# Kernel optimization log

Hardware: AMD Instinct MI355X
Metric: run time of the kernel (lower is better)

## Reference

```python
import jax, jax.numpy as jnp
import numpy as np
import math

NUM_HEADS = 32
NUM_KV_HEADS = 8
HEAD_DIM = 64
ROPE_THETA = 150000.0


def rotate_half(x):
    half = x.shape[-1] // 2
    return jnp.concatenate([-x[..., half:], x[..., :half]], axis=-1)


def setup_inputs() -> dict:
    key = jax.random.key(0)
    k1, k2, k3, k4, k5 = jax.random.split(key, 5)
    B, S, H = 2, 2048, 2048
    qkv_size = (NUM_HEADS + 2 * NUM_KV_HEADS) * HEAD_DIM  # 3072
    scale = 1.0 / math.sqrt(H)
    return {
        "hidden_states": jax.random.normal(k1, (B, S, H), jnp.float32),
        "position_ids": jnp.arange(S, dtype=jnp.int64 if jax.config.jax_enable_x64 else jnp.int32)[None, :],
        "qkv_w": jax.random.normal(k2, (qkv_size, H), jnp.float32) * scale,
        "qkv_b": jax.random.normal(k3, (qkv_size,), jnp.float32) * 0.01,
        "o_w": jax.random.normal(k4, (H, NUM_HEADS * HEAD_DIM), jnp.float32) * scale,
        "o_b": jax.random.normal(k5, (H,), jnp.float32) * 0.01,
    }


def reference(hidden_states, position_ids, qkv_w, qkv_b, o_w, o_b):
    B, S, _ = hidden_states.shape
    g = NUM_HEADS // NUM_KV_HEADS  # query heads per kv head
    d = HEAD_DIM

    qkv = hidden_states @ qkv_w.T + qkv_b  # [B,S,(H+2KV)*d]
    qkv = qkv.reshape(B, S, NUM_KV_HEADS, g + 2, d)
    q = qkv[:, :, :, :g, :].reshape(B, S, NUM_HEADS, d).transpose(0, 2, 1, 3)   # [B,Hq,S,d]
    k = qkv[:, :, :, g, :].transpose(0, 2, 1, 3)                                 # [B,Hkv,S,d]
    v = qkv[:, :, :, g + 1, :].transpose(0, 2, 1, 3)                             # [B,Hkv,S,d]

    # HF-style RoPE: cos/sin [S, d]
    inv_freq = 1.0 / (ROPE_THETA ** (jnp.arange(0, d, 2, dtype=jnp.float32) / d))
    freqs = jnp.outer(position_ids.reshape(-1).astype(jnp.float32), inv_freq)    # [S, d/2]
    emb = jnp.concatenate([freqs, freqs], axis=-1)                               # [S, d]
    cos = jnp.cos(emb)[None, None]                                               # [1,1,S,d]
    sin = jnp.sin(emb)[None, None]
    q = q * cos + rotate_half(q) * sin
    k = k * cos + rotate_half(k) * sin

    # GQA: repeat_interleave kv heads to match query heads
    k = jnp.repeat(k, g, axis=1)  # [B,Hq,S,d]
    v = jnp.repeat(v, g, axis=1)

    scores = jnp.einsum("bhqd,bhkd->bhqk", q, k) / math.sqrt(d)  # [B,Hq,S,S]
    attn = jax.nn.softmax(scores, axis=-1)
    out = jnp.einsum("bhqk,bhkd->bhqd", attn, v)
    out = out.transpose(0, 2, 1, 3).reshape(B, S, NUM_HEADS * d)
    return out @ o_w.T + o_b
```

## Files before the change

kernel.cpp:

```cpp
#include <hip/hip_runtime.h>
#include <math.h>

#define NHQ 32
#define NKV 8
#define HD 64
#define QKV_DIM 3072
#define MODEL_DIM 2048
#define QSCALE 0.1803368801111204f

typedef __attribute__((ext_vector_type(4))) float     f32x4;
typedef __attribute__((ext_vector_type(8))) _Float16  half8;
typedef __attribute__((ext_vector_type(4))) _Float16  half4v;
typedef __attribute__((ext_vector_type(2))) __fp16    fp16x2;
typedef __attribute__((ext_vector_type(4))) unsigned  uint32x4;

#define ASYNC_COPY16(g, l)                                                        \
    __builtin_amdgcn_global_load_lds(                                             \
        (const __attribute__((address_space(1))) void*)(g),                       \
        (__attribute__((address_space(3))) void*)(l), 16, 0, 0)

__device__ __forceinline__ float fast_exp2(float x)
{
#if __has_builtin(__builtin_amdgcn_exp2f)
    return __builtin_amdgcn_exp2f(x);
#else
    float r;
    asm volatile("v_exp_f32 %0, %1\ns_nop 0" : "=v"(r) : "v"(x));
    return r;
#endif
}

__global__ __launch_bounds__(256)
void f32_to_f16_kernel(const float* __restrict__ src, _Float16* __restrict__ dst, int n4)
{
    int i = blockIdx.x * 256 + threadIdx.x;
    if (i < n4) {
        float4 v = ((const float4*)src)[i];
        half4v h = { (_Float16)v.x, (_Float16)v.y, (_Float16)v.z, (_Float16)v.w };
        ((half4v*)dst)[i] = h;
    }
}

__global__ __launch_bounds__(256)
void sincos_table_kernel(const int* __restrict__ pos, float* __restrict__ tab, int S)
{
    int i = blockIdx.x * 256 + threadIdx.x;
    if (i < S * 32) {
        int s = i >> 5, fi = i & 31;
        float p = (float)pos[s];
        float inv_freq = powf(150000.0f, -(float)fi * (1.0f / 32.0f));
        float ang = p * inv_freq;
        tab[s * 64 + fi]      = cosf(ang);
        tab[s * 64 + 32 + fi] = sinf(ang);
    }
}

template<int MODE>
__global__ __launch_bounds__(512, 2)
void gemm_f16_mfma(const _Float16* __restrict__ A, const _Float16* __restrict__ W,
                   const float* __restrict__ bias, void* __restrict__ Cout,
                   const float* __restrict__ tab, int M, int N, int K, int S)
{
    __shared__ _Float16 As[3][128 * 32];
    __shared__ _Float16 Bs[3][256 * 32];

    const int t    = threadIdx.x;
    const int w    = t >> 6;
    const int lane = t & 63;
    const int quad = lane >> 4, l15 = lane & 15;
    const size_t m0 = (size_t)blockIdx.y * 128;
    const size_t n0 = (size_t)blockIdx.x * 256;
    const int wm = (w >> 2) * 64;
    const int wn = (w & 3) * 64;

    const int sr   = t >> 2;
    const int klog = ((t & 3) ^ ((sr >> 1) & 3)) * 8;
    const _Float16* ag0 = A + (m0 + sr) * K + klog;
    const _Float16* bg0 = W + (n0 + sr) * K + klog;
    const _Float16* bg1 = W + (n0 + 128 + sr) * K + klog;

    const int xk8 = (quad ^ ((l15 >> 1) & 3)) * 8;

    f32x4 acc[4][4];
#pragma unroll
    for (int i = 0; i < 4; i++)
#pragma unroll
        for (int j = 0; j < 4; j++) acc[i][j] = (f32x4){0.f, 0.f, 0.f, 0.f};

    const int nkt = K >> 5;

#define STAGE_TILE(bi, kt_)                                         \
    do {                                                            \
        const int _k0 = (kt_) * 32;                                 \
        ASYNC_COPY16(ag0 + _k0, &As[bi][w * 512]);                  \
        ASYNC_COPY16(bg0 + _k0, &Bs[bi][w * 512]);                  \
        ASYNC_COPY16(bg1 + _k0, &Bs[bi][4096 + w * 512]);           \
    } while (0)

    STAGE_TILE(0, 0);
    STAGE_TILE(1, 1);
    asm volatile("s_waitcnt vmcnt(3)" ::: "memory");
    __builtin_amdgcn_s_barrier();
    __builtin_amdgcn_sched_barrier(0);

    int bc = 0;
    for (int kt = 0; kt < nkt; ++kt) {
        const _Float16* Ab = &As[bc][0];
        const _Float16* Bb = &Bs[bc][0];

        half8 af[4], bf[4];
#pragma unroll
        for (int i = 0; i < 4; i++) {
            af[i] = *(const half8*)(Ab + (wm + i * 16 + l15) * 32 + xk8);
            bf[i] = *(const half8*)(Bb + (wn + i * 16 + l15) * 32 + xk8);
        }

        if (kt + 2 < nkt) {
            int bs = bc + 2; if (bs >= 3) bs -= 3;
            STAGE_TILE(bs, kt + 2);
        }

        __builtin_amdgcn_s_setprio(1);
#pragma unroll
        for (int i = 0; i < 4; i++)
#pragma unroll
            for (int j = 0; j < 4; j++)
                acc[i][j] = __builtin_amdgcn_mfma_f32_16x16x32_f16(af[i], bf[j], acc[i][j], 0, 0, 0);
        __builtin_amdgcn_s_setprio(0);

        if (kt + 1 < nkt) {
            if (kt + 2 < nkt) asm volatile("s_waitcnt vmcnt(3)" ::: "memory");
            else              asm volatile("s_waitcnt vmcnt(0)" ::: "memory");
            __builtin_amdgcn_s_barrier();
            __builtin_amdgcn_sched_barrier(0);
        }
        bc = bc + 1; if (bc == 3) bc = 0;
    }
#undef STAGE_TILE

    float bv[4];
#pragma unroll
    for (int j = 0; j < 4; j++) bv[j] = bias[n0 + wn + j * 16 + l15];

    const int ct = (int)(((n0 + wn) >> 6) % 6);

#pragma unroll
    for (int i = 0; i < 4; i++)
#pragma unroll
        for (int r = 0; r < 4; r++) {
            const size_t row = m0 + wm + i * 16 + quad * 4 + r;
            float v[4];
#pragma unroll
            for (int j = 0; j < 4; j++) v[j] = acc[i][j][r] + bv[j];

            if (MODE == 2 && ct != 5) {
                const float* tc = tab + (size_t)(row % S) * 64;
                const float ca = tc[l15],      sa = tc[32 + l15];
                const float cb = tc[16 + l15], sb = tc[48 + l15];
                const float qs = (ct < 4) ? QSCALE : 1.0f;
                const float n0v = v[0] * ca - v[2] * sa;
                const float n1v = v[1] * cb - v[3] * sb;
                const float n2v = v[2] * ca + v[0] * sa;
                const float n3v = v[3] * cb + v[1] * sb;
                v[0] = n0v * qs; v[1] = n1v * qs; v[2] = n2v * qs; v[3] = n3v * qs;
            }

            const size_t col = n0 + wn + l15;
#pragma unroll
            for (int j = 0; j < 4; j++) {
                if (MODE != 0) ((_Float16*)Cout)[row * N + col + j * 16] = (_Float16)v[j];
                else           ((float*)Cout)[row * N + col + j * 16] = v[j];
            }
        }
}

__global__ __launch_bounds__(256)
void transpose_v_kernel(const _Float16* __restrict__ qkv, _Float16* __restrict__ vtg, int BS)
{
    __shared__ _Float16 tile[64 * 72];
    const int t = threadIdx.x;
    const int tb = blockIdx.x * 64;
    const int g = blockIdx.y;
    const int voff = (g * 6 + 5) * 64;

    const int tok = t >> 2, dsub = (t & 3) * 16;
    const _Float16* src = qkv + (size_t)(tb + tok) * QKV_DIM + voff + dsub;
    *(half8*)&tile[tok * 72 + dsub]     = *(const half8*)(src);
    *(half8*)&tile[tok * 72 + dsub + 8] = *(const half8*)(src + 8);
    __syncthreads();

    const int d = t >> 2, tsub = (t & 3) * 16;
    half8 a, c;
#pragma unroll
    for (int i = 0; i < 8; i++) a[i] = tile[(tsub + i) * 72 + d];
#pragma unroll
    for (int i = 0; i < 8; i++) c[i] = tile[(tsub + 8 + i) * 72 + d];
    _Float16* dst = vtg + ((size_t)g * 64 + d) * BS + tb + tsub;
    *(half8*)dst       = a;
    *(half8*)(dst + 8) = c;
}

__global__ __launch_bounds__(256)
void attn_mfma(const _Float16* __restrict__ qkv, const _Float16* __restrict__ vtg,
               _Float16* __restrict__ out, int B, int S)
{
    __shared__ _Float16 Ks[64 * 72];
    __shared__ _Float16 VsT[64 * 72];

    const int t = threadIdx.x, w = t >> 6, lane = t & 63;
    const int quad = lane >> 4, l15 = lane & 15;
    const int b = blockIdx.z, g = blockIdx.y;
    const int q0 = blockIdx.x * 32;
    const int qoff = (g * 6 + w) * 64;
    const int koff = (g * 6 + 4) * 64;

    half8 qf[2][2];
#pragma unroll
    for (int s = 0; s < 2; s++) {
        const _Float16* qp = qkv + (size_t)(b * S + q0 + s * 16 + l15) * QKV_DIM + qoff;
        qf[s][0] = *(const half8*)(qp + quad * 8);
        qf[s][1] = *(const half8*)(qp + 32 + quad * 8);
    }

    half8 lv;
    {
        const _Float16 one = (l15 == 0) ? (_Float16)1.0f : (_Float16)0.0f;
#pragma unroll
        for (int j = 0; j < 8; j++) lv[j] = one;
    }

    f32x4 O[2][4], L[2];
#pragma unroll
    for (int s = 0; s < 2; s++) {
        L[s] = (f32x4){0.f, 0.f, 0.f, 0.f};
#pragma unroll
        for (int dt = 0; dt < 4; dt++) O[s][dt] = (f32x4){0.f, 0.f, 0.f, 0.f};
    }

    const int kst_tok = t >> 2;
    const int kst_d   = (t & 3) * 16;
    const int vst_d   = t >> 3;
    const int vst_sub = (t & 7) * 8;

    const _Float16* kbase  = qkv + (size_t)(b * S + kst_tok) * QKV_DIM + koff + kst_d;
    const _Float16* vbase0 = vtg + ((size_t)g * 64 + vst_d) * (size_t)(B * S) + b * S + vst_sub;
    const _Float16* vbase1 = vtg + ((size_t)g * 64 + 32 + vst_d) * (size_t)(B * S) + b * S + vst_sub;

    half8 kr0 = *(const half8*)(kbase);
    half8 kr1 = *(const half8*)(kbase + 8);
    half8 vr0 = *(const half8*)(vbase0);
    half8 vr1 = *(const half8*)(vbase1);

    for (int kt = 0; kt < S; kt += 64) {
        *(half8*)&Ks[kst_tok * 72 + kst_d]         = kr0;
        *(half8*)&Ks[kst_tok * 72 + kst_d + 8]     = kr1;
        *(half8*)&VsT[vst_d * 72 + vst_sub]        = vr0;
        *(half8*)&VsT[(32 + vst_d) * 72 + vst_sub] = vr1;
        __syncthreads();

        if (kt + 64 < S) {
            kr0 = *(const half8*)(kbase + (size_t)(kt + 64) * QKV_DIM);
            kr1 = *(const half8*)(kbase + (size_t)(kt + 64) * QKV_DIM + 8);
            vr0 = *(const half8*)(vbase0 + kt + 64);
            vr1 = *(const half8*)(vbase1 + kt + 64);
        }

        half8 kf[4][2];
#pragma unroll
        for (int mt = 0; mt < 4; mt++) {
            kf[mt][0] = *(const half8*)&Ks[(mt * 16 + l15) * 72 + quad * 8];
            kf[mt][1] = *(const half8*)&Ks[(mt * 16 + l15) * 72 + 32 + quad * 8];
        }

        half8 pf[2][2];
#pragma unroll
        for (int s = 0; s < 2; s++) {
            f32x4 sacc[4];
#pragma unroll
            for (int mt = 0; mt < 4; mt++) {
                f32x4 z = (f32x4){0.f, 0.f, 0.f, 0.f};
                z = __builtin_amdgcn_mfma_f32_16x16x32_f16(kf[mt][0], qf[s][0], z, 0, 0, 0);
                z = __builtin_amdgcn_mfma_f32_16x16x32_f16(kf[mt][1], qf[s][1], z, 0, 0, 0);
                sacc[mt] = z;
            }

            unsigned u[4][2];
#pragma unroll
            for (int mt = 0; mt < 4; mt++) {
                fp16x2 pa = __builtin_amdgcn_cvt_pkrtz(fast_exp2(sacc[mt][0]),
                                                       fast_exp2(sacc[mt][1]));
                fp16x2 pb = __builtin_amdgcn_cvt_pkrtz(fast_exp2(sacc[mt][2]),
                                                       fast_exp2(sacc[mt][3]));
                u[mt][0] = __builtin_bit_cast(unsigned, pa);
                u[mt][1] = __builtin_bit_cast(unsigned, pb);
            }

#pragma unroll
            for (int h = 0; h < 2; h++) {
                uint32x4 pw;
#pragma unroll
                for (int c = 0; c < 2; c++) {
                    unsigned x = u[h * 2][c], y = u[h * 2 + 1][c];
                    asm("v_permlane32_swap_b32 %0, %1" : "+v"(x), "+v"(y));
                    asm("v_permlane16_swap_b32 %0, %1" : "+v"(x), "+v"(y));
                    pw[c]     = x;
                    pw[2 + c] = y;
                }
                pf[s][h] = __builtin_bit_cast(half8, pw);
            }
        }

#pragma unroll
        for (int dt = 0; dt < 4; dt++) {
            half8 vv0 = *(const half8*)&VsT[(dt * 16 + l15) * 72 + quad * 8];
            half8 vv1 = *(const half8*)&VsT[(dt * 16 + l15) * 72 + 32 + quad * 8];
#pragma unroll
            for (int s = 0; s < 2; s++) {
                O[s][dt] = __builtin_amdgcn_mfma_f32_16x16x32_f16(pf[s][0], vv0, O[s][dt], 0, 0, 0);
                O[s][dt] = __builtin_amdgcn_mfma_f32_16x16x32_f16(pf[s][1], vv1, O[s][dt], 0, 0, 0);
            }
        }
#pragma unroll
        for (int s = 0; s < 2; s++) {
            L[s] = __builtin_amdgcn_mfma_f32_16x16x32_f16(pf[s][0], lv, L[s], 0, 0, 0);
            L[s] = __builtin_amdgcn_mfma_f32_16x16x32_f16(pf[s][1], lv, L[s], 0, 0, 0);
        }
        __syncthreads();
    }

    const int hq = g * 4 + w;
#pragma unroll
    for (int s = 0; s < 2; s++)
#pragma unroll
        for (int r = 0; r < 4; r++) {
            const float lr = __shfl(L[s][r], lane & 48, 64);
            const float ir = 1.0f / lr;
            const size_t row = (size_t)(b * S + q0 + s * 16 + quad * 4 + r);
#pragma unroll
            for (int dt = 0; dt < 4; dt++)
                out[row * (NHQ * HD) + hq * 64 + dt * 16 + l15] = (_Float16)(O[s][dt][r] * ir);
        }
}

extern "C" void kernel_launch(void* const* d_in, const int* in_sizes, int n_in,
                              void* d_out, int out_size, void* d_ws, size_t ws_size,
                              hipStream_t stream)
{
    const float* hidden = (const float*)d_in[0];
    const int*   pos    = (const int*)d_in[1];
    const float* qkv_w  = (const float*)d_in[2];
    const float* qkv_b  = (const float*)d_in[3];
    const float* o_w    = (const float*)d_in[4];
    const float* o_b    = (const float*)d_in[5];
    float* out = (float*)d_out;

    const int S  = in_sizes[1];
    const int BS = in_sizes[0] / MODEL_DIM;
    const int B  = BS / S;

    _Float16* hA   = (_Float16*)d_ws;
    _Float16* hW1  = hA   + (size_t)BS * MODEL_DIM;
    _Float16* hW2  = hW1  + (size_t)QKV_DIM * MODEL_DIM;
    _Float16* qkvh = hW2  + (size_t)MODEL_DIM * MODEL_DIM;
    _Float16* atth = qkvh + (size_t)BS * QKV_DIM;
    float*    tab  = (float*)(atth + (size_t)BS * MODEL_DIM);
    _Float16* vtg  = (_Float16*)(tab + (size_t)S * 64);

    f32_to_f16_kernel<<<(BS * MODEL_DIM / 4 + 255) / 256, 256, 0, stream>>>(hidden, hA, BS * MODEL_DIM / 4);
    f32_to_f16_kernel<<<(QKV_DIM * MODEL_DIM / 4 + 255) / 256, 256, 0, stream>>>(qkv_w, hW1, QKV_DIM * MODEL_DIM / 4);
    f32_to_f16_kernel<<<(MODEL_DIM * MODEL_DIM / 4 + 255) / 256, 256, 0, stream>>>(o_w, hW2, MODEL_DIM * MODEL_DIM / 4);
    sincos_table_kernel<<<(S * 32 + 255) / 256, 256, 0, stream>>>(pos, tab, S);

    gemm_f16_mfma<2><<<dim3(QKV_DIM / 256, BS / 128), 512, 0, stream>>>(
        hA, hW1, qkv_b, qkvh, tab, BS, QKV_DIM, MODEL_DIM, S);

    transpose_v_kernel<<<dim3(BS / 64, NKV), 256, 0, stream>>>(qkvh, vtg, BS);

    attn_mfma<<<dim3(S / 32, NKV, B), 256, 0, stream>>>(qkvh, vtg, atth, B, S);

    gemm_f16_mfma<0><<<dim3(MODEL_DIM / 256, BS / 128), 512, 0, stream>>>(
        atth, hW2, o_b, out, nullptr, BS, MODEL_DIM, MODEL_DIM, S);
}
```

Before: 315.7 us.

## Enlarge GEMM tile to 256x256x64 with phased double-buffered staging; fuse prep kernels

New measurement: 339.5 us. +7.6%, slower.

```diff
diff --git a/kernel.cpp b/kernel.cpp
--- a/kernel.cpp
+++ b/kernel.cpp
@@ -31,27 +31,30 @@
 }
 
 __global__ __launch_bounds__(256)
-void f32_to_f16_kernel(const float* __restrict__ src, _Float16* __restrict__ dst, int n4)
-{
-    int i = blockIdx.x * 256 + threadIdx.x;
-    if (i < n4) {
-        float4 v = ((const float4*)src)[i];
+void prep_kernel(const float* __restrict__ s0, _Float16* __restrict__ d0, int n0,
+                 const float* __restrict__ s1, _Float16* __restrict__ d1, int n1,
+                 const float* __restrict__ s2, _Float16* __restrict__ d2, int n2,
+                 const int* __restrict__ pos, float* __restrict__ tab, int ns)
+{
+    int j = blockIdx.x * 256 + threadIdx.x;
+    if (j < n0 + n1 + n2) {
+        const float* s; _Float16* d;
+        if (j < n0)           { s = s0; d = d0; }
+        else if (j < n0 + n1) { s = s1; d = d1; j -= n0; }
+        else                  { s = s2; d = d2; j -= n0 + n1; }
+        float4 v = ((const float4*)s)[j];
         half4v h = { (_Float16)v.x, (_Float16)v.y, (_Float16)v.z, (_Float16)v.w };
-        ((half4v*)dst)[i] = h;
-    }
-}
-
-__global__ __launch_bounds__(256)
-void sincos_table_kernel(const int* __restrict__ pos, float* __restrict__ tab, int S)
-{
-    int i = blockIdx.x * 256 + threadIdx.x;
-    if (i < S * 32) {
-        int s = i >> 5, fi = i & 31;
-        float p = (float)pos[s];
-        float inv_freq = powf(150000.0f, -(float)fi * (1.0f / 32.0f));
-        float ang = p * inv_freq;
-        tab[s * 64 + fi]      = cosf(ang);
-        tab[s * 64 + 32 + fi] = sinf(ang);
+        ((half4v*)d)[j] = h;
+    } else {
+        j -= n0 + n1 + n2;
+        if (j < ns) {
+            int s = j >> 5, fi = j & 31;
+            float p = (float)pos[s];
+            float inv_freq = powf(150000.0f, -(float)fi * (1.0f / 32.0f));
+            float ang = p * inv_freq;
+            tab[s * 64 + fi]      = cosf(ang);
+            tab[s * 64 + 32 + fi] = sinf(ang);
+        }
     }
 }
 
@@ -61,82 +64,138 @@
                    const float* __restrict__ bias, void* __restrict__ Cout,
                    const float* __restrict__ tab, int M, int N, int K, int S)
 {
-    __shared__ _Float16 As[3][128 * 32];
-    __shared__ _Float16 Bs[3][256 * 32];
+    __shared__ _Float16 As[2][256 * 64];
+    __shared__ _Float16 Bs[2][256 * 64];
 
     const int t    = threadIdx.x;
     const int w    = t >> 6;
     const int lane = t & 63;
     const int quad = lane >> 4, l15 = lane & 15;
-    const size_t m0 = (size_t)blockIdx.y * 128;
+    const size_t m0 = (size_t)blockIdx.y * 256;
     const size_t n0 = (size_t)blockIdx.x * 256;
-    const int wm = (w >> 2) * 64;
+    const int wm = (w >> 2) * 128;
     const int wn = (w & 3) * 64;
 
-    const int sr   = t >> 2;
-    const int klog = ((t & 3) ^ ((sr >> 1) & 3)) * 8;
-    const _Float16* ag0 = A + (m0 + sr) * K + klog;
-    const _Float16* bg0 = W + (n0 + sr) * K + klog;
-    const _Float16* bg1 = W + (n0 + 128 + sr) * K + klog;
-
-    const int xk8 = (quad ^ ((l15 >> 1) & 3)) * 8;
-
-    f32x4 acc[4][4];
-#pragma unroll
-    for (int i = 0; i < 4; i++)
+    const int srow = w * 8 + (lane >> 3);
+    const int sco  = ((lane & 7) ^ ((lane >> 3) & 7)) << 3;
+    const _Float16* aS = A + (m0 + srow) * K + sco;
+    const _Float16* bS = W + (n0 + srow) * K + sco;
+
+    const int xsel = l15 & 7;
+
+    f32x4 acc[8][4];
+#pragma unroll
+    for (int i = 0; i < 8; i++)
 #pragma unroll
         for (int j = 0; j < 4; j++) acc[i][j] = (f32x4){0.f, 0.f, 0.f, 0.f};
 
-    const int nkt = K >> 5;
-
-#define STAGE_TILE(bi, kt_)                                         \
-    do {                                                            \
-        const int _k0 = (kt_) * 32;                                 \
-        ASYNC_COPY16(ag0 + _k0, &As[bi][w * 512]);                  \
-        ASYNC_COPY16(bg0 + _k0, &Bs[bi][w * 512]);                  \
-        ASYNC_COPY16(bg1 + _k0, &Bs[bi][4096 + w * 512]);           \
+    const int NT = K >> 6;
+
+#define STG_A(bi, T_, p) ASYNC_COPY16(aS + (size_t)(64 * (p)) * K + (T_) * 64,    \
+                                      &As[bi][((p) * 512 + w * 64) * 8])
+#define STG_B(bi, T_, p) ASYNC_COPY16(bS + (size_t)(64 * (p)) * K + (T_) * 64,    \
+                                      &Bs[bi][((p) * 512 + w * 64) * 8])
+
+#define LDA(cur, QM)                                                              \
+    do {                                                                          \
+        _Pragma("unroll")                                                         \
+        for (int i = 0; i < 4; i++) {                                             \
+            _Pragma("unroll")                                                     \
+            for (int kk = 0; kk < 2; kk++)                                        \
+                fa[i][kk] = *(const half8*)&As[cur][                              \
+                    (wm + ((QM) * 4 + i) * 16 + l15) * 64 +                       \
+                    ((kk * 4 + quad) ^ xsel) * 8];                                \
+        }                                                                         \
     } while (0)
 
-    STAGE_TILE(0, 0);
-    STAGE_TILE(1, 1);
-    asm volatile("s_waitcnt vmcnt(3)" ::: "memory");
+#define LDB(cur, J0)                                                              \
+    do {                                                                          \
+        _Pragma("unroll")                                                         \
+        for (int jj = 0; jj < 2; jj++) {                                          \
+            _Pragma("unroll")                                                     \
+            for (int kk = 0; kk < 2; kk++)                                        \
+                fb[(J0) + jj][kk] = *(const half8*)&Bs[cur][                      \
+                    (wn + ((J0) + jj) * 16 + l15) * 64 +                          \
+                    ((kk * 4 + quad) ^ xsel) * 8];                                \
+        }                                                                         \
+    } while (0)
+
+#define MM16(QM, J0)                                                              \
+    do {                                                                          \
+        __builtin_amdgcn_s_setprio(1);                                            \
+        _Pragma("unroll")                                                         \
+        for (int i = 0; i < 4; i++)                                               \
+            _Pragma("unroll")                                                     \
+            for (int jj = 0; jj < 2; jj++)                                        \
+                _Pragma("unroll")                                                 \
+                for (int kk = 0; kk < 2; kk++)                                    \
+                    acc[(QM) * 4 + i][(J0) + jj] =                                \
+                        __builtin_amdgcn_mfma_f32_16x16x32_f16(                   \
+                            fa[i][kk], fb[(J0) + jj][kk],                         \
+                            acc[(QM) * 4 + i][(J0) + jj], 0, 0, 0);               \
+        __builtin_amdgcn_s_setprio(0);                                            \
+    } while (0)
+
+#define PHASE_SYNC                                                                \
+    do {                                                                          \
+        __builtin_amdgcn_sched_barrier(0);                                        \
+        __builtin_amdgcn_s_barrier();                                             \
+        asm volatile("s_waitcnt lgkmcnt(0)" ::: "memory");                        \
+        __builtin_amdgcn_sched_barrier(0);                                        \
+    } while (0)
+
+    STG_A(0, 0, 0); STG_A(0, 0, 1); STG_A(0, 0, 2); STG_A(0, 0, 3);
+    STG_B(0, 0, 0); STG_B(0, 0, 1); STG_B(0, 0, 2); STG_B(0, 0, 3);
+    if (NT > 1) {
+        STG_A(1, 1, 0); STG_A(1, 1, 2);
+        asm volatile("s_waitcnt vmcnt(2)" ::: "memory");
+    } else {
+        asm volatile("s_waitcnt vmcnt(0)" ::: "memory");
+    }
     __builtin_amdgcn_s_barrier();
     __builtin_amdgcn_sched_barrier(0);
 
-    int bc = 0;
-    for (int kt = 0; kt < nkt; ++kt) {
-        const _Float16* Ab = &As[bc][0];
-        const _Float16* Bb = &Bs[bc][0];
-
-        half8 af[4], bf[4];
-#pragma unroll
-        for (int i = 0; i < 4; i++) {
-            af[i] = *(const half8*)(Ab + (wm + i * 16 + l15) * 32 + xk8);
-            bf[i] = *(const half8*)(Bb + (wn + i * 16 + l15) * 32 + xk8);
-        }
-
-        if (kt + 2 < nkt) {
-            int bs = bc + 2; if (bs >= 3) bs -= 3;
-            STAGE_TILE(bs, kt + 2);
-        }
-
-        __builtin_amdgcn_s_setprio(1);
-#pragma unroll
-        for (int i = 0; i < 4; i++)
-#pragma unroll
-            for (int j = 0; j < 4; j++)
-                acc[i][j] = __builtin_amdgcn_mfma_f32_16x16x32_f16(af[i], bf[j], acc[i][j], 0, 0, 0);
-        __builtin_amdgcn_s_setprio(0);
-
-        if (kt + 1 < nkt) {
-            if (kt + 2 < nkt) asm volatile("s_waitcnt vmcnt(3)" ::: "memory");
-            else              asm volatile("s_waitcnt vmcnt(0)" ::: "memory");
+    half8 fa[4][2], fb[4][2];
+
+    for (int T = 0; T < NT; ++T) {
+        const int cur = T & 1;
+        const int nxt = cur ^ 1;
+
+        LDA(cur, 0);
+        LDB(cur, 0);
+        if (T + 1 < NT) { STG_A(nxt, T + 1, 1); STG_A(nxt, T + 1, 3); }
+        PHASE_SYNC;
+        MM16(0, 0);
+        __builtin_amdgcn_s_barrier();
+
+        LDB(cur, 2);
+        if (T + 1 < NT) { STG_B(nxt, T + 1, 0); STG_B(nxt, T + 1, 1); }
+        PHASE_SYNC;
+        MM16(0, 2);
+        __builtin_amdgcn_s_barrier();
+
+        LDA(cur, 1);
+        if (T + 1 < NT) { STG_B(nxt, T + 1, 2); STG_B(nxt, T + 1, 3); }
+        PHASE_SYNC;
+        MM16(1, 0);
+        __builtin_amdgcn_s_barrier();
+
+        if (T + 2 < NT) { STG_A(cur, T + 2, 0); STG_A(cur, T + 2, 2); }
+        __builtin_amdgcn_sched_barrier(0);
+        MM16(1, 2);
+        if (T + 1 < NT) {
+            if (T + 2 < NT) asm volatile("s_waitcnt vmcnt(2)" ::: "memory");
+            else            asm volatile("s_waitcnt vmcnt(0)" ::: "memory");
             __builtin_amdgcn_s_barrier();
             __builtin_amdgcn_sched_barrier(0);
         }
-        bc = bc + 1; if (bc == 3) bc = 0;
-    }
-#undef STAGE_TILE
+    }
+#undef STG_A
+#undef STG_B
+#undef LDA
+#undef LDB
+#undef MM16
+#undef PHASE_SYNC
 
     float bv[4];
 #pragma unroll
@@ -145,7 +204,7 @@
     const int ct = (int)(((n0 + wn) >> 6) % 6);
 
 #pragma unroll
-    for (int i = 0; i < 4; i++)
+    for (int i = 0; i < 8; i++)
 #pragma unroll
         for (int r = 0; r < 4; r++) {
             const size_t row = m0 + wm + i * 16 + quad * 4 + r;
@@ -366,18 +425,20 @@
     float*    tab  = (float*)(atth + (size_t)BS * MODEL_DIM);
     _Float16* vtg  = (_Float16*)(tab + (size_t)S * 64);
 
-    f32_to_f16_kernel<<<(BS * MODEL_DIM / 4 + 255) / 256, 256, 0, stream>>>(hidden, hA, BS * MODEL_DIM / 4);
-    f32_to_f16_kernel<<<(QKV_DIM * MODEL_DIM / 4 + 255) / 256, 256, 0, stream>>>(qkv_w, hW1, QKV_DIM * MODEL_DIM / 4);
-    f32_to_f16_kernel<<<(MODEL_DIM * MODEL_DIM / 4 + 255) / 256, 256, 0, stream>>>(o_w, hW2, MODEL_DIM * MODEL_DIM / 4);
-    sincos_table_kernel<<<(S * 32 + 255) / 256, 256, 0, stream>>>(pos, tab, S);
-
-    gemm_f16_mfma<2><<<dim3(QKV_DIM / 256, BS / 128), 512, 0, stream>>>(
+    const int n0 = BS * MODEL_DIM / 4;
+    const int n1 = QKV_DIM * MODEL_DIM / 4;
+    const int n2 = MODEL_DIM * MODEL_DIM / 4;
+    const int ns = S * 32;
+    prep_kernel<<<(n0 + n1 + n2 + ns + 255) / 256, 256, 0, stream>>>(
+        hidden, hA, n0, qkv_w, hW1, n1, o_w, hW2, n2, pos, tab, ns);
+
+    gemm_f16_mfma<2><<<dim3(QKV_DIM / 256, BS / 256), 512, 0, stream>>>(
         hA, hW1, qkv_b, qkvh, tab, BS, QKV_DIM, MODEL_DIM, S);
 
     transpose_v_kernel<<<dim3(BS / 64, NKV), 256, 0, stream>>>(qkvh, vtg, BS);
 
     attn_mfma<<<dim3(S / 32, NKV, B), 256, 0, stream>>>(qkvh, vtg, atth, B, S);
 
-    gemm_f16_mfma<0><<<dim3(MODEL_DIM / 256, BS / 128), 512, 0, stream>>>(
+    gemm_f16_mfma<0><<<dim3(MODEL_DIM / 256, BS / 256), 512, 0, stream>>>(
         atth, hW2, o_b, out, nullptr, BS, MODEL_DIM, MODEL_DIM, S);
 }
```
